# Optimization experiments

Measured on AMD Instinct MI355X. Metric: run time of the kernel, lower is better.

## Reference

```python
import jax, jax.numpy as jnp
import numpy as np


def setup_inputs() -> dict:
    key = jax.random.key(0)
    prediction = jax.random.normal(key, (16, 4096), dtype=jnp.float32)
    return {"prediction": prediction}


def reference(prediction):
    # prediction: [B, N]
    B, N = prediction.shape
    ntriu_elem = jnp.asarray(N * (N - 1) / 2, dtype=prediction.dtype)
    # pairwise_diff[b, i, j] = pred[b, i] - pred[b, j]  -> [B, N, N]
    pairwise_diff = prediction[:, :, None] - prediction[:, None, :]
    # torch.triu keeps j >= i (upper triangle incl. diagonal; diag is zero anyway)
    triu_mask = jnp.triu(jnp.ones((N, N), dtype=bool))  # [N, N]
    triu = jnp.where(triu_mask, pairwise_diff, jnp.zeros((), dtype=prediction.dtype))
    avg_diff = jnp.abs(triu).sum(axis=-1) / ntriu_elem  # [B, N]
    return avg_diff.mean()
```

## Files before the change

### kernel.cpp

```cpp
#include <hip/hip_runtime.h>


#define NN      4096
#define THREADS 256
#define WAVES   4
#define R       4
#define CSZ     256
#define JSEG    128
#define UPR     272
#define BPR     68

__global__ __launch_bounds__(THREADS) void pairdist_part(
    const float* __restrict__ pred, float* __restrict__ partials)
{
    const int lane = threadIdx.x & 63;
    const int wid  = threadIdx.x >> 6;
    const int b    = blockIdx.x / BPR;
    int u = (blockIdx.x % BPR) * WAVES + wid;

    int c = 0;
    while (u >= 32 - 2 * c) { u -= 32 - 2 * c; ++c; }
    const int   jh = 2 * c + u;
    const float w  = (u < 2) ? 0.5f : 1.0f;

    const float* __restrict__ row = pred + (size_t)b * NN;

    __shared__ float sj[WAVES][JSEG];
    sj[wid][lane]      = row[jh * JSEG + lane];
    sj[wid][64 + lane] = row[jh * JSEG + 64 + lane];

    float pi[R];
#pragma unroll
    for (int k = 0; k < R; ++k)
        pi[k] = row[c * CSZ + k * 64 + lane];

    __syncthreads();

    float a0 = 0.f, a1 = 0.f, a2 = 0.f, a3 = 0.f;
#pragma unroll 8
    for (int j = 0; j < JSEG; j += 4) {
        float4 jv = *reinterpret_cast<const float4*>(&sj[wid][j]);
        a0 += fabsf(pi[0] - jv.x); a1 += fabsf(pi[1] - jv.x);
        a2 += fabsf(pi[2] - jv.x); a3 += fabsf(pi[3] - jv.x);
        a0 += fabsf(pi[0] - jv.y); a1 += fabsf(pi[1] - jv.y);
        a2 += fabsf(pi[2] - jv.y); a3 += fabsf(pi[3] - jv.y);
        a0 += fabsf(pi[0] - jv.z); a1 += fabsf(pi[1] - jv.z);
        a2 += fabsf(pi[2] - jv.z); a3 += fabsf(pi[3] - jv.z);
        a0 += fabsf(pi[0] - jv.w); a1 += fabsf(pi[1] - jv.w);
        a2 += fabsf(pi[2] - jv.w); a3 += fabsf(pi[3] - jv.w);
    }
    float s = (a0 + a1) + (a2 + a3);

#pragma unroll
    for (int off = 32; off > 0; off >>= 1)
        s += __shfl_down(s, off, 64);

    if (lane == 0)
        partials[blockIdx.x * WAVES + wid] = s * w;
}

__global__ __launch_bounds__(64) void pairdist_fin(
    const float* __restrict__ partials, float* __restrict__ out, double scale)
{
    double s = 0.0;
#pragma unroll
    for (int cc = 0; cc < 17; ++cc) {
        float4 v = *reinterpret_cast<const float4*>(
            &partials[(cc * 64 + threadIdx.x) * 4]);
        s += ((double)v.x + (double)v.y) + ((double)v.z + (double)v.w);
    }
#pragma unroll
    for (int off = 32; off > 0; off >>= 1)
        s += __shfl_down(s, off, 64);
    if (threadIdx.x == 0) out[0] = (float)(s * scale);
}

extern "C" void kernel_launch(void* const* d_in, const int* in_sizes, int n_in,
                              void* d_out, int out_size, void* d_ws, size_t ws_size,
                              hipStream_t stream) {
    const float* pred = (const float*)d_in[0];
    const int total = in_sizes[0];
    const int B = total / NN;
    const int nblocks = B * BPR;

    float* partials = (float*)d_ws;

    pairdist_part<<<nblocks, THREADS, 0, stream>>>(pred, partials);

    const double ntriu = (double)NN * (double)(NN - 1) * 0.5;
    const double scale = 1.0 / (ntriu * (double)B * (double)NN);
    pairdist_fin<<<1, 64, 0, stream>>>(partials, (float*)d_out, scale);
}
```

Measured before the change: 18.16 us.

## Fuse partial and final reduction into one kernel via tagged-slot spin wait

Merges the two-kernel reduction into a single launch. Block 0 acts as the finalizer: 64 threads poll tagged 64-bit slots until every compute block has published its block-level sum, then reduce in double and write the output. Each compute block first combines its four wave sums through shared memory into one slot value. Afterwards the finalizer clears the tags so the next call starts clean. This removes the second kernel launch and the gap between kernels. In exchange it depends on block 0 staying resident while the other blocks make progress, and on the workspace never holding a stale tag on the first call.

```diff
diff --git a/kernel.cpp b/kernel.cpp
--- a/kernel.cpp
+++ b/kernel.cpp
@@ -7,16 +7,56 @@
 #define R       4
 #define CSZ     256
 #define JSEG    128
-#define UPR     272
 #define BPR     68
+#define NSLOT   1088
+#define MAGIC   0x7F3A9C51u
 
-__global__ __launch_bounds__(THREADS) void pairdist_part(
-    const float* __restrict__ pred, float* __restrict__ partials)
+__global__ __launch_bounds__(THREADS) void pairdist_fused(
+    const float* __restrict__ pred,
+    unsigned long long* __restrict__ slots,
+    float* __restrict__ out, double scale)
 {
+    if (blockIdx.x == 0) {
+        if (threadIdx.x >= 64) return;
+        const int l = threadIdx.x;
+        float vals[17];
+        unsigned seen = 0;
+        while (seen != 0x1FFFFu) {
+#pragma unroll
+            for (int k = 0; k < 17; ++k) {
+                if (!(seen & (1u << k))) {
+                    unsigned long long p = __hip_atomic_load(
+                        &slots[l + 64 * k], __ATOMIC_RELAXED,
+                        __HIP_MEMORY_SCOPE_AGENT);
+                    if ((unsigned)(p >> 32) == MAGIC) {
+                        vals[k] = __uint_as_float((unsigned)p);
+                        seen |= 1u << k;
+                    }
+                }
+            }
+            __builtin_amdgcn_s_sleep(2);
+        }
+        double s = 0.0;
+#pragma unroll
+        for (int k = 0; k < 17; ++k) s += (double)vals[k];
+#pragma unroll
+        for (int off = 32; off > 0; off >>= 1)
+            s += __shfl_down(s, off, 64);
+        if (l == 0) out[0] = (float)(s * scale);
+#pragma unroll
+        for (int k = 0; k < 17; ++k) {
+            unsigned* tag = ((unsigned*)&slots[l + 64 * k]) + 1;
+            __hip_atomic_store(tag, 0u, __ATOMIC_RELAXED,
+                               __HIP_MEMORY_SCOPE_AGENT);
+        }
+        return;
+    }
+
+    const int cb   = blockIdx.x - 1;
     const int lane = threadIdx.x & 63;
     const int wid  = threadIdx.x >> 6;
-    const int b    = blockIdx.x / BPR;
-    int u = (blockIdx.x % BPR) * WAVES + wid;
+    const int b    = cb / BPR;
+    int u = (cb % BPR) * WAVES + wid;
 
     int c = 0;
     while (u >= 32 - 2 * c) { u -= 32 - 2 * c; ++c; }
@@ -26,6 +66,7 @@
     const float* __restrict__ row = pred + (size_t)b * NN;
 
     __shared__ float sj[WAVES][JSEG];
+    __shared__ float sw[WAVES];
     sj[wid][lane]      = row[jh * JSEG + lane];
     sj[wid][64 + lane] = row[jh * JSEG + 64 + lane];
 
@@ -33,8 +74,6 @@
 #pragma unroll
     for (int k = 0; k < R; ++k)
         pi[k] = row[c * CSZ + k * 64 + lane];
-
-    __syncthreads();
 
     float a0 = 0.f, a1 = 0.f, a2 = 0.f, a3 = 0.f;
 #pragma unroll 8
@@ -55,24 +94,16 @@
     for (int off = 32; off > 0; off >>= 1)
         s += __shfl_down(s, off, 64);
 
-    if (lane == 0)
-        partials[blockIdx.x * WAVES + wid] = s * w;
-}
+    if (lane == 0) sw[wid] = s * w;
+    __syncthreads();
 
-__global__ __launch_bounds__(64) void pairdist_fin(
-    const float* __restrict__ partials, float* __restrict__ out, double scale)
-{
-    double s = 0.0;
-#pragma unroll
-    for (int cc = 0; cc < 17; ++cc) {
-        float4 v = *reinterpret_cast<const float4*>(
-            &partials[(cc * 64 + threadIdx.x) * 4]);
-        s += ((double)v.x + (double)v.y) + ((double)v.z + (double)v.w);
+    if (threadIdx.x == 0) {
+        float bs = (sw[0] + sw[1]) + (sw[2] + sw[3]);
+        unsigned long long p = ((unsigned long long)MAGIC << 32) |
+                               (unsigned long long)__float_as_uint(bs);
+        __hip_atomic_store(&slots[cb], p, __ATOMIC_RELAXED,
+                           __HIP_MEMORY_SCOPE_AGENT);
     }
-#pragma unroll
-    for (int off = 32; off > 0; off >>= 1)
-        s += __shfl_down(s, off, 64);
-    if (threadIdx.x == 0) out[0] = (float)(s * scale);
 }
 
 extern "C" void kernel_launch(void* const* d_in, const int* in_sizes, int n_in,
@@ -81,13 +112,13 @@
     const float* pred = (const float*)d_in[0];
     const int total = in_sizes[0];
     const int B = total / NN;
-    const int nblocks = B * BPR;
+    const int nblocks = 1 + B * BPR;
 
-    float* partials = (float*)d_ws;
-
-    pairdist_part<<<nblocks, THREADS, 0, stream>>>(pred, partials);
+    unsigned long long* slots = (unsigned long long*)d_ws;
 
     const double ntriu = (double)NN * (double)(NN - 1) * 0.5;
     const double scale = 1.0 / (ntriu * (double)B * (double)NN);
-    pairdist_fin<<<1, 64, 0, stream>>>(partials, (float*)d_out, scale);
+
+    pairdist_fused<<<nblocks, THREADS, 0, stream>>>(
+        pred, slots, (float*)d_out, scale);
 }
```

Result: no change. 18.01 us (-0.8%).
